# Optimization experiments

Hardware: AMD Instinct MI355X
Metric: run time of the kernel (lower is better)

The kernel has to match this reference:

```python
import jax, jax.numpy as jnp
import numpy as np

PATCH_SIZE = 16
PATCH_STRIDE = 8
LEVEL = 3

# pywt db4 decomposition filters (dec_lo, dec_hi)
_DB4_DEC_LO = np.array([-0.010597401784997278, 0.032883011666982945,
                        0.030841381835986965, -0.18703481171888114,
                        -0.02798376941698385, 0.6308807679295904,
                        0.7148465705525415, 0.23037781330885523], dtype=np.float32)
_DB4_DEC_HI = np.array([-0.23037781330885523, 0.7148465705525415,
                        -0.6308807679295904, -0.02798376941698385,
                        0.18703481171888114, 0.030841381835986965,
                        -0.032883011666982945, -0.010597401784997278], dtype=np.float32)


def _swt(x, level):
    """Undecimated (a-trous) SWT with periodic boundary, ptwt convention.
    x: (BN, T) with T divisible by 2**level. Returns [cA_L, cD_L, ..., cD_1]."""
    # torch conv1d is cross-correlation -> use flipped filters (true convolution)
    filt = jnp.stack([jnp.asarray(_DB4_DEC_LO[::-1].copy()),
                      jnp.asarray(_DB4_DEC_HI[::-1].copy())], axis=0)[:, None, :]  # (2,1,8)
    filt = filt.astype(x.dtype)
    flen = filt.shape[-1]
    res_lo = x[:, None, :]  # (BN, 1, T)
    details = []
    for lvl in range(level):
        d = 2 ** lvl
        padl, padr = d * (flen // 2 - 1), d * (flen // 2)
        xp = jnp.concatenate([res_lo[..., -padl:], res_lo, res_lo[..., :padr]], axis=-1)
        res = jax.lax.conv_general_dilated(
            xp, filt, window_strides=(1,), padding='VALID',
            rhs_dilation=(d,), dimension_numbers=('NCH', 'OIH', 'NCH'))  # (BN,2,T)
        res_lo = res[:, :1, :]
        details.append(res[:, 1, :])
    return [res_lo[:, 0, :]] + details[::-1]


def setup_inputs() -> dict:
    key = jax.random.key(0)
    x = jax.random.normal(key, (64, 4096, 32), dtype=jnp.float32)
    return {"x": x}


def reference(x):
    B, T, N = x.shape
    xt = jnp.transpose(x, (0, 2, 1))  # (B, N, T)
    pow2 = 2 ** LEVEL
    pad_len = (-T) % pow2
    if pad_len:
        xt = jnp.pad(xt, ((0, 0), (0, 0), (0, pad_len)), mode='edge')  # replicate
    T_pad = T + pad_len
    coeffs = _swt(xt.reshape(B * N, T_pad), LEVEL)           # (level+1) x (BN, T_pad)
    cs = jnp.stack(coeffs, axis=1).reshape(B, N, LEVEL + 1, T_pad)
    if pad_len:
        cs = cs[..., :T]
    P = (T - PATCH_SIZE) // PATCH_STRIDE + 1
    idx = jnp.arange(P)[:, None] * PATCH_STRIDE + jnp.arange(PATCH_SIZE)[None, :]
    patches = cs[..., idx]                                   # (B, N, L+1, P, p)
    patches = jnp.transpose(patches, (0, 3, 1, 2, 4))        # (B, P, N, L+1, p)
    return patches.reshape(B * P, N * (LEVEL + 1), PATCH_SIZE)
```

## Files before the change

### kernel.cpp

```cpp
#include <hip/hip_runtime.h>


#define NTHREADS 256
#define T_MASK   4095

#define S_IN  132
#define S_A1  116
#define S_A2  108
#define S_ST  76
#define OFF_IN 0
#define OFF_A1 4224
#define OFF_A2 0
#define OFF_ST 7936
#define ST_C   2436
#define LDS_FLOATS (OFF_ST + 4*ST_C)

__device__ __constant__ float c_lo[8] = {
    -0.010597401784997278f, 0.032883011666982945f, 0.030841381835986965f,
    -0.18703481171888114f, -0.02798376941698385f, 0.6308807679295904f,
    0.7148465705525415f,   0.23037781330885523f};
__device__ __constant__ float c_hi[8] = {
    -0.23037781330885523f, 0.7148465705525415f, -0.6308807679295904f,
    -0.02798376941698385f, 0.18703481171888114f, 0.030841381835986965f,
    -0.032883011666982945f, -0.010597401784997278f};

__global__ __launch_bounds__(NTHREADS, 2) void swt_patch(const float* __restrict__ x,
                                                         float* __restrict__ out) {
    __shared__ float lds[LDS_FLOATS];

    const int blk = blockIdx.x;
    const int b   = blk >> 6;
    const int cid = blk & 63;
    const int T0  = cid << 6;
    const int p0  = cid << 3;
    const int tid = threadIdx.x;

    const float* xb = x + (size_t)b * (4096 * 32);
    {
#pragma unroll
        for (int it = 0; it < 4; ++it) {
            const int id = tid + it * NTHREADS;
            const int i  = id >> 3;
            const int n0 = (id & 7) * 4;
            const int t  = (T0 - 23 + i) & T_MASK;
            const float4 v = *(const float4*)&xb[(size_t)t * 32 + n0];
            lds[OFF_IN + (n0 + 0) * S_IN + i] = v.x;
            lds[OFF_IN + (n0 + 1) * S_IN + i] = v.y;
            lds[OFF_IN + (n0 + 2) * S_IN + i] = v.z;
            lds[OFF_IN + (n0 + 3) * S_IN + i] = v.w;
        }
    }
    __syncthreads();

    for (int tsk = tid; tsk < 29 * 32; tsk += NTHREADS) {
        const int n = tsk & 31, q = tsk >> 5;
        const int trel0 = -20 + 4 * q;
        float w[12];
        const int base = OFF_IN + n * S_IN + 4 * q;
        *(float4*)&w[0] = *(const float4*)&lds[base];
        *(float4*)&w[4] = *(const float4*)&lds[base + 4];
        *(float4*)&w[8] = *(const float4*)&lds[base + 8];
        float4 va, vd;
        float* pa = (float*)&va; float* pd = (float*)&vd;
#pragma unroll
        for (int ii = 0; ii < 4; ++ii) {
            float sa = 0.f, sd = 0.f;
#pragma unroll
            for (int j = 0; j < 8; ++j) {
                const float v = w[ii + 7 - j];
                sa = fmaf(c_lo[j], v, sa);
                sd = fmaf(c_hi[j], v, sd);
            }
            pa[ii] = sa; pd[ii] = sd;
        }
        *(float4*)&lds[OFF_A1 + n * S_A1 + (trel0 + 20)] = va;
        if (trel0 >= 0 && trel0 <= 68)
            *(float4*)&lds[OFF_ST + 3 * ST_C + n * S_ST + trel0] = vd;
    }
    __syncthreads();

    for (int tsk = tid; tsk < 25 * 32; tsk += NTHREADS) {
        const int n = tsk & 31, q = tsk >> 5;
        const int trel0 = -12 + 4 * q;
        float w[20];
        const int base = OFF_A1 + n * S_A1 + 4 * q;
#pragma unroll
        for (int c4 = 0; c4 < 5; ++c4)
            *(float4*)&w[4 * c4] = *(const float4*)&lds[base + 4 * c4];
        float4 va, vd;
        float* pa = (float*)&va; float* pd = (float*)&vd;
#pragma unroll
        for (int ii = 0; ii < 4; ++ii) {
            float sa = 0.f, sd = 0.f;
#pragma unroll
            for (int j = 0; j < 8; ++j) {
                const float v = w[ii + 16 - 2 * j];
                sa = fmaf(c_lo[j], v, sa);
                sd = fmaf(c_hi[j], v, sd);
            }
            pa[ii] = sa; pd[ii] = sd;
        }
        *(float4*)&lds[OFF_A2 + n * S_A2 + (trel0 + 12)] = va;
        if (trel0 >= 0 && trel0 <= 68)
            *(float4*)&lds[OFF_ST + 2 * ST_C + n * S_ST + trel0] = vd;
    }
    __syncthreads();

    for (int tsk = tid; tsk < 18 * 32; tsk += NTHREADS) {
        const int n = tsk & 31, q = tsk >> 5;
        const int trel0 = 4 * q;
        float w[32];
        const int base = OFF_A2 + n * S_A2 + trel0;
#pragma unroll
        for (int c4 = 0; c4 < 8; ++c4)
            *(float4*)&w[4 * c4] = *(const float4*)&lds[base + 4 * c4];
        float4 va, vd;
        float* pa = (float*)&va; float* pd = (float*)&vd;
#pragma unroll
        for (int ii = 0; ii < 4; ++ii) {
            float sa = 0.f, sd = 0.f;
#pragma unroll
            for (int j = 0; j < 8; ++j) {
                const float v = w[ii + 28 - 4 * j];
                sa = fmaf(c_lo[j], v, sa);
                sd = fmaf(c_hi[j], v, sd);
            }
            pa[ii] = sa; pd[ii] = sd;
        }
        *(float4*)&lds[OFF_ST + 0 * ST_C + n * S_ST + trel0] = va;
        *(float4*)&lds[OFF_ST + 1 * ST_C + n * S_ST + trel0] = vd;
    }
    __syncthreads();

    float4* out4 = (float4*)(out + ((size_t)b * 511 + p0) * 2048);
#pragma unroll
    for (int it = 0; it < 16; ++it) {
        const int e4 = tid + it * NTHREADS;
        const int p_local = e4 >> 9;
        if (p0 + p_local < 511) {
            const int n  = (e4 >> 4) & 31;
            const int c  = (e4 >> 2) & 3;
            const int trel = 8 * p_local + 4 * (e4 & 3);
            out4[e4] = *(const float4*)&lds[OFF_ST + c * ST_C + n * S_ST + trel];
        }
    }
}

extern "C" void kernel_launch(void* const* d_in, const int* in_sizes, int n_in,
                              void* d_out, int out_size, void* d_ws, size_t ws_size,
                              hipStream_t stream) {
    const float* x = (const float*)d_in[0];
    float* out = (float*)d_out;
    hipLaunchKernelGGL(swt_patch, dim3(64 * 64), dim3(NTHREADS), 0, stream, x, out);
}
```

Baseline: 290.4 us.

## Fuse level-3 SWT with direct patch output and drop staging buffer

Each thread now computes a full 16-sample patch of level-3 approximation and detail for one channel in registers, reads level-1/2 details from LDS, and writes its 256-byte output row straight to global memory with nontemporal stores. This removes the level-3 staging writes, one barrier, and the separate LDS-to-global copy loop, and cuts LDS size enough to raise the occupancy hint to 3 blocks. In exchange, overlapping patches make level-3 work redundant (about 2x), register pressure rises (w[44] plus coef[64]), and per-thread stores stride 256 bytes apart, which hurts coalescing.

Result: slower. 845.4 us (+191.1%).

```diff
diff --git a/kernel.cpp b/kernel.cpp
--- a/kernel.cpp
+++ b/kernel.cpp
@@ -3,6 +3,8 @@
 
 #define NTHREADS 256
 #define T_MASK   4095
+
+typedef float floatx4 __attribute__((ext_vector_type(4)));
 
 #define S_IN  132
 #define S_A1  116
@@ -11,9 +13,9 @@
 #define OFF_IN 0
 #define OFF_A1 4224
 #define OFF_A2 0
-#define OFF_ST 7936
-#define ST_C   2436
-#define LDS_FLOATS (OFF_ST + 4*ST_C)
+#define OFF_D1 7936
+#define OFF_D2 10368
+#define LDS_FLOATS 12800
 
 __device__ __constant__ float c_lo[8] = {
     -0.010597401784997278f, 0.032883011666982945f, 0.030841381835986965f,
@@ -24,7 +26,7 @@
     -0.02798376941698385f, 0.18703481171888114f, 0.030841381835986965f,
     -0.032883011666982945f, -0.010597401784997278f};
 
-__global__ __launch_bounds__(NTHREADS, 2) void swt_patch(const float* __restrict__ x,
+__global__ __launch_bounds__(NTHREADS, 3) void swt_patch(const float* __restrict__ x,
                                                          float* __restrict__ out) {
     __shared__ float lds[LDS_FLOATS];
 
@@ -36,19 +38,17 @@
     const int tid = threadIdx.x;
 
     const float* xb = x + (size_t)b * (4096 * 32);
-    {
 #pragma unroll
-        for (int it = 0; it < 4; ++it) {
-            const int id = tid + it * NTHREADS;
-            const int i  = id >> 3;
-            const int n0 = (id & 7) * 4;
-            const int t  = (T0 - 23 + i) & T_MASK;
-            const float4 v = *(const float4*)&xb[(size_t)t * 32 + n0];
-            lds[OFF_IN + (n0 + 0) * S_IN + i] = v.x;
-            lds[OFF_IN + (n0 + 1) * S_IN + i] = v.y;
-            lds[OFF_IN + (n0 + 2) * S_IN + i] = v.z;
-            lds[OFF_IN + (n0 + 3) * S_IN + i] = v.w;
-        }
+    for (int it = 0; it < 4; ++it) {
+        const int id = tid + it * NTHREADS;
+        const int i  = id >> 3;
+        const int n0 = (id & 7) * 4;
+        const int t  = (T0 - 23 + i) & T_MASK;
+        const floatx4 v = *(const floatx4*)&xb[(size_t)t * 32 + n0];
+        lds[OFF_IN + (n0 + 0) * S_IN + i] = v.x;
+        lds[OFF_IN + (n0 + 1) * S_IN + i] = v.y;
+        lds[OFF_IN + (n0 + 2) * S_IN + i] = v.z;
+        lds[OFF_IN + (n0 + 3) * S_IN + i] = v.w;
     }
     __syncthreads();
 
@@ -57,11 +57,10 @@
         const int trel0 = -20 + 4 * q;
         float w[12];
         const int base = OFF_IN + n * S_IN + 4 * q;
-        *(float4*)&w[0] = *(const float4*)&lds[base];
-        *(float4*)&w[4] = *(const float4*)&lds[base + 4];
-        *(float4*)&w[8] = *(const float4*)&lds[base + 8];
-        float4 va, vd;
-        float* pa = (float*)&va; float* pd = (float*)&vd;
+        *(floatx4*)&w[0] = *(const floatx4*)&lds[base];
+        *(floatx4*)&w[4] = *(const floatx4*)&lds[base + 4];
+        *(floatx4*)&w[8] = *(const floatx4*)&lds[base + 8];
+        floatx4 va, vd;
 #pragma unroll
         for (int ii = 0; ii < 4; ++ii) {
             float sa = 0.f, sd = 0.f;
@@ -71,11 +70,11 @@
                 sa = fmaf(c_lo[j], v, sa);
                 sd = fmaf(c_hi[j], v, sd);
             }
-            pa[ii] = sa; pd[ii] = sd;
+            va[ii] = sa; vd[ii] = sd;
         }
-        *(float4*)&lds[OFF_A1 + n * S_A1 + (trel0 + 20)] = va;
+        *(floatx4*)&lds[OFF_A1 + n * S_A1 + (trel0 + 20)] = va;
         if (trel0 >= 0 && trel0 <= 68)
-            *(float4*)&lds[OFF_ST + 3 * ST_C + n * S_ST + trel0] = vd;
+            *(floatx4*)&lds[OFF_D1 + n * S_ST + trel0] = vd;
     }
     __syncthreads();
 
@@ -86,9 +85,8 @@
         const int base = OFF_A1 + n * S_A1 + 4 * q;
 #pragma unroll
         for (int c4 = 0; c4 < 5; ++c4)
-            *(float4*)&w[4 * c4] = *(const float4*)&lds[base + 4 * c4];
-        float4 va, vd;
-        float* pa = (float*)&va; float* pd = (float*)&vd;
+            *(floatx4*)&w[4 * c4] = *(const floatx4*)&lds[base + 4 * c4];
+        floatx4 va, vd;
 #pragma unroll
         for (int ii = 0; ii < 4; ++ii) {
             float sa = 0.f, sd = 0.f;
@@ -98,50 +96,46 @@
                 sa = fmaf(c_lo[j], v, sa);
                 sd = fmaf(c_hi[j], v, sd);
             }
-            pa[ii] = sa; pd[ii] = sd;
+            va[ii] = sa; vd[ii] = sd;
         }
-        *(float4*)&lds[OFF_A2 + n * S_A2 + (trel0 + 12)] = va;
+        *(floatx4*)&lds[OFF_A2 + n * S_A2 + (trel0 + 12)] = va;
         if (trel0 >= 0 && trel0 <= 68)
-            *(float4*)&lds[OFF_ST + 2 * ST_C + n * S_ST + trel0] = vd;
+            *(floatx4*)&lds[OFF_D2 + n * S_ST + trel0] = vd;
     }
     __syncthreads();
 
-    for (int tsk = tid; tsk < 18 * 32; tsk += NTHREADS) {
-        const int n = tsk & 31, q = tsk >> 5;
-        const int trel0 = 4 * q;
-        float w[32];
-        const int base = OFF_A2 + n * S_A2 + trel0;
+    {
+        const int n = tid & 31, p = tid >> 5;
+        float w[44];
+        const int base = OFF_A2 + n * S_A2 + 8 * p;
 #pragma unroll
-        for (int c4 = 0; c4 < 8; ++c4)
-            *(float4*)&w[4 * c4] = *(const float4*)&lds[base + 4 * c4];
-        float4 va, vd;
-        float* pa = (float*)&va; float* pd = (float*)&vd;
+        for (int c4 = 0; c4 < 11; ++c4)
+            *(floatx4*)&w[4 * c4] = *(const floatx4*)&lds[base + 4 * c4];
+
+        float coef[64];
 #pragma unroll
-        for (int ii = 0; ii < 4; ++ii) {
+        for (int jj = 0; jj < 16; ++jj) {
             float sa = 0.f, sd = 0.f;
 #pragma unroll
             for (int j = 0; j < 8; ++j) {
-                const float v = w[ii + 28 - 4 * j];
+                const float v = w[jj + 28 - 4 * j];
                 sa = fmaf(c_lo[j], v, sa);
                 sd = fmaf(c_hi[j], v, sd);
             }
-            pa[ii] = sa; pd[ii] = sd;
+            coef[jj]      = sa;
+            coef[16 + jj] = sd;
         }
-        *(float4*)&lds[OFF_ST + 0 * ST_C + n * S_ST + trel0] = va;
-        *(float4*)&lds[OFF_ST + 1 * ST_C + n * S_ST + trel0] = vd;
-    }
-    __syncthreads();
-
-    float4* out4 = (float4*)(out + ((size_t)b * 511 + p0) * 2048);
+        const int sbase = n * S_ST + 8 * p;
 #pragma unroll
-    for (int it = 0; it < 16; ++it) {
-        const int e4 = tid + it * NTHREADS;
-        const int p_local = e4 >> 9;
-        if (p0 + p_local < 511) {
-            const int n  = (e4 >> 4) & 31;
-            const int c  = (e4 >> 2) & 3;
-            const int trel = 8 * p_local + 4 * (e4 & 3);
-            out4[e4] = *(const float4*)&lds[OFF_ST + c * ST_C + n * S_ST + trel];
+        for (int c4 = 0; c4 < 4; ++c4) {
+            *(floatx4*)&coef[32 + 4 * c4] = *(const floatx4*)&lds[OFF_D2 + sbase + 4 * c4];
+            *(floatx4*)&coef[48 + 4 * c4] = *(const floatx4*)&lds[OFF_D1 + sbase + 4 * c4];
+        }
+        if (p0 + p < 511) {
+            floatx4* dst = (floatx4*)(out + ((size_t)b * 511 + p0 + p) * 2048 + n * 64);
+#pragma unroll
+            for (int s = 0; s < 16; ++s)
+                __builtin_nontemporal_store(*(const floatx4*)&coef[4 * s], dst + s);
         }
     }
 }
```
